# Kernel optimization log

Hardware: AMD Instinct MI355X
Metric: run time of the kernel (lower is better)

Reference implementation:

```python
import jax, jax.numpy as jnp
import numpy as np

INIT_RANGE = 0.02


def setup_inputs() -> dict:
    key = jax.random.key(0)
    ks = jax.random.split(key, 7)
    B, S, E, H, D = 4, 2048, 1024, 16, 64
    return {
        "query": jax.random.normal(ks[0], (B, S, E), dtype=jnp.float32),
        "key": jax.random.normal(ks[1], (B, S, E), dtype=jnp.float32),
        "value": jax.random.normal(ks[2], (B, S, E), dtype=jnp.float32),
        "W_Q": jax.random.normal(ks[3], (H, E, D), dtype=jnp.float32) * INIT_RANGE,
        "W_K": jax.random.normal(ks[4], (H, E, D), dtype=jnp.float32) * INIT_RANGE,
        "W_V": jax.random.normal(ks[5], (H, E, D), dtype=jnp.float32) * INIT_RANGE,
        "W_O": jax.random.normal(ks[6], (H, D, E), dtype=jnp.float32) * INIT_RANGE,
        "b_Q": jnp.zeros((H, D), dtype=jnp.float32),
        "b_K": jnp.zeros((H, D), dtype=jnp.float32),
        "b_V": jnp.zeros((H, D), dtype=jnp.float32),
        "b_O": jnp.zeros((E,), dtype=jnp.float32),
    }


def reference(query, key, value, W_Q, W_K, W_V, W_O, b_Q, b_K, b_V, b_O):
    head_dim = W_Q.shape[-1]
    scale = 1.0 / jnp.sqrt(jnp.asarray(head_dim, dtype=query.dtype))
    # Per-head projections: [B,S,E] x [H,E,D] -> [B,S,H,D]
    Q = jnp.einsum('bse,hed->bshd', query, W_Q) + b_Q
    K = jnp.einsum('bse,hed->bshd', key, W_K) + b_K
    V = jnp.einsum('bse,hed->bshd', value, W_V) + b_V
    # Scores: [B,H,S_from,S_to]
    scores = jnp.einsum('bfhd,bthd->bhft', Q, K) * scale
    attn = jax.nn.softmax(scores, axis=-1)
    # Weighted values: [B,H,S,D]
    OV = jnp.einsum('bhft,bthd->bhfd', attn, V)
    # Output projection: [B,S,E]
    return jnp.einsum('bhsd,hde->bse', OV, W_O) + b_O
```

## Files before the change

kernel.cpp:

```cpp
#include <hip/hip_runtime.h>
#include <hip/hip_bf16.h>

typedef __attribute__((ext_vector_type(8))) short bf16x8;
typedef __attribute__((ext_vector_type(4))) float f32x4;
typedef __attribute__((ext_vector_type(16))) float f32x16;
typedef __attribute__((ext_vector_type(4))) int i32x4;

#define LOG2E 1.4426950408889634f

__device__ __forceinline__ short f2bf(float f){
  unsigned u = __float_as_uint(f);
  u += 0x7fffu + ((u >> 16) & 1u);
  return (short)(u >> 16);
}
__device__ __forceinline__ unsigned cvtpk(float lo, float hi){
  unsigned r;
  asm("v_cvt_pk_bf16_f32 %0, %1, %2" : "=v"(r) : "v"(lo), "v"(hi));
  return r;
}
__device__ __forceinline__ void plswap(unsigned &a, unsigned &b){
  asm("v_permlane32_swap_b32 %0, %1" : "+v"(a), "+v"(b));
}
__device__ __forceinline__ void gl_lds16(const short* g, short* l){
  __builtin_amdgcn_global_load_lds((const __attribute__((address_space(1))) void*)g,
                                   (__attribute__((address_space(3))) void*)l, 16, 0, 0);
}

__global__ __launch_bounds__(256) void prep_wqkv3(const float* __restrict__ Wq,
                                                  const float* __restrict__ Wk,
                                                  const float* __restrict__ Wv,
                                                  short* __restrict__ WqT,
                                                  short* __restrict__ WkT,
                                                  short* __restrict__ WvT){
  __shared__ short t[64][72];
  int h = blockIdx.x >> 4, et = blockIdx.x & 15;
  int tid = threadIdx.x;
  int er = tid >> 2, qc = (tid & 3) * 16;
  #pragma unroll
  for (int a = 0; a < 3; ++a){
    const float* W = a == 0 ? Wq : (a == 1 ? Wk : Wv);
    short* Wt = a == 0 ? WqT : (a == 1 ? WkT : WvT);
    if (a) __syncthreads();
    const float* src = W + h * 65536 + (et * 64 + er) * 64 + qc;
    #pragma unroll
    for (int v = 0; v < 4; ++v){
      float4 f = *(const float4*)(src + v * 4);
      t[qc + v * 4 + 0][er] = f2bf(f.x);
      t[qc + v * 4 + 1][er] = f2bf(f.y);
      t[qc + v * 4 + 2][er] = f2bf(f.z);
      t[qc + v * 4 + 3][er] = f2bf(f.w);
    }
    __syncthreads();
    bf16x8 o0 = *(const bf16x8*)&t[er][qc];
    bf16x8 o1 = *(const bf16x8*)&t[er][qc + 8];
    size_t dst = (size_t)(h * 64 + er) * 1024 + et * 64 + qc;
    *(bf16x8*)&Wt[dst] = o0;
    *(bf16x8*)&Wt[dst + 8] = o1;
  }
}
__global__ __launch_bounds__(256) void prep_wo(const float* __restrict__ W, short* __restrict__ Wt){
  __shared__ short t[64][72];
  int bi = blockIdx.x >> 4, bj = blockIdx.x & 15;
  int tid = threadIdx.x;
  int r = tid >> 2, qc = (tid & 3) * 16;
  const float* src = W + (size_t)(bi * 64 + r) * 1024 + bj * 64 + qc;
  #pragma unroll
  for (int v = 0; v < 4; ++v){
    float4 f = *(const float4*)(src + v * 4);
    t[qc + v * 4 + 0][r] = f2bf(f.x);
    t[qc + v * 4 + 1][r] = f2bf(f.y);
    t[qc + v * 4 + 2][r] = f2bf(f.z);
    t[qc + v * 4 + 3][r] = f2bf(f.w);
  }
  __syncthreads();
  bf16x8 o0 = *(const bf16x8*)&t[r][qc];
  bf16x8 o1 = *(const bf16x8*)&t[r][qc + 8];
  size_t dst = (size_t)(bj * 64 + r) * 1024 + bi * 64 + qc;
  *(bf16x8*)&Wt[dst] = o0;
  *(bf16x8*)&Wt[dst + 8] = o1;
}
__global__ __launch_bounds__(256) void xconv3(const float* __restrict__ xq,
                                              const float* __restrict__ xk,
                                              const float* __restrict__ xv,
                                              short* __restrict__ oq,
                                              short* __restrict__ ok,
                                              short* __restrict__ ov){
  int idx = (blockIdx.x * 256 + threadIdx.x) * 8;
  #pragma unroll
  for (int a = 0; a < 3; ++a){
    const float* x = a == 0 ? xq : (a == 1 ? xk : xv);
    short* o = a == 0 ? oq : (a == 1 ? ok : ov);
    float4 v0 = *(const float4*)&x[idx];
    float4 v1 = *(const float4*)&x[idx + 4];
    bf16x8 t;
    t[0]=f2bf(v0.x); t[1]=f2bf(v0.y); t[2]=f2bf(v0.z); t[3]=f2bf(v0.w);
    t[4]=f2bf(v1.x); t[5]=f2bf(v1.y); t[6]=f2bf(v1.z); t[7]=f2bf(v1.w);
    *(bf16x8*)&o[idx] = t;
  }
}

__global__ __launch_bounds__(256) void proj_gemm(const short* __restrict__ A,
                                                 const short* __restrict__ Wt,
                                                 const float* __restrict__ bias,
                                                 short* __restrict__ Out,
                                                 float scale){
  __shared__ short Al[128][64];
  __shared__ short Bl[128][64];
  int tid = threadIdx.x;
  int bm0 = blockIdx.x * 128, bn0 = blockIdx.y * 128;
  int w = tid >> 6, lane = tid & 63;
  int wm = w >> 1, wn = w & 1;
  int r16 = lane & 15, kblk = lane >> 4;
  int srow = tid >> 3, schunk = tid & 7;

  f32x4 acc[4][4] = {};
  for (int kt = 0; kt < 16; ++kt){
    int k0 = kt * 64;
    __syncthreads();
    #pragma unroll
    for (int p = 0; p < 4; ++p){
      int row = p * 32 + srow;
      int sc = (schunk ^ (row & 7)) * 8;
      gl_lds16(A  + (size_t)(bm0 + row) * 1024 + k0 + sc, &Al[p * 32 + w * 8][0]);
      gl_lds16(Wt + (size_t)(bn0 + row) * 1024 + k0 + sc, &Bl[p * 32 + w * 8][0]);
    }
    __syncthreads();
    bf16x8 af[2][4], bfr[2][4];
    #pragma unroll
    for (int half = 0; half < 2; ++half){
      #pragma unroll
      for (int m = 0; m < 4; ++m){
        int r = wm * 64 + m * 16 + r16;
        af[half][m] = *(bf16x8*)&Al[r][(((half << 2) | kblk) ^ (r & 7)) * 8];
      }
      #pragma unroll
      for (int n = 0; n < 4; ++n){
        int r = wn * 64 + n * 16 + r16;
        bfr[half][n] = *(bf16x8*)&Bl[r][(((half << 2) | kblk) ^ (r & 7)) * 8];
      }
    }
    #pragma unroll
    for (int half = 0; half < 2; ++half)
      #pragma unroll
      for (int m = 0; m < 4; ++m)
        #pragma unroll
        for (int n = 0; n < 4; ++n)
          acc[m][n] = __builtin_amdgcn_mfma_f32_16x16x32_bf16(af[half][m], bfr[half][n], acc[m][n], 0, 0, 0);
  }
  #pragma unroll
  for (int m = 0; m < 4; ++m){
    int grow0 = bm0 + wm * 64 + m * 16 + kblk * 4;
    #pragma unroll
    for (int n = 0; n < 4; ++n){
      int gcol = bn0 + wn * 64 + n * 16 + r16;
      float bv = bias[gcol];
      int h = gcol >> 6, d = gcol & 63;
      #pragma unroll
      for (int i = 0; i < 4; ++i){
        int grow = grow0 + i;
        int b = grow >> 11, s = grow & 2047;
        Out[(size_t)((b * 16 + h) * 2048 + s) * 64 + d] = f2bf((acc[m][n][i] + bv) * scale);
      }
    }
  }
}

__global__ __launch_bounds__(256) void out_gemm(const short* __restrict__ A,
                                                const short* __restrict__ Wt,
                                                const float* __restrict__ bias,
                                                float* __restrict__ Out){
  __shared__ short Al[128][64];
  __shared__ short Bl[128][64];
  int tid = threadIdx.x;
  int bm0 = blockIdx.x * 128, bn0 = blockIdx.y * 128;
  int w = tid >> 6, lane = tid & 63;
  int wm = w >> 1, wn = w & 1;
  int r16 = lane & 15, kblk = lane >> 4;
  int srow = tid >> 3, schunk = tid & 7;
  f32x4 acc[4][4] = {};
  for (int kt = 0; kt < 16; ++kt){
    int k0 = kt * 64;
    __syncthreads();
    #pragma unroll
    for (int p = 0; p < 4; ++p){
      int row = p * 32 + srow;
      int sc = (schunk ^ (row & 7)) * 8;
      gl_lds16(A  + (size_t)(bm0 + row) * 1024 + k0 + sc, &Al[p * 32 + w * 8][0]);
      gl_lds16(Wt + (size_t)(bn0 + row) * 1024 + k0 + sc, &Bl[p * 32 + w * 8][0]);
    }
    __syncthreads();
    bf16x8 af[2][4], bfr[2][4];
    #pragma unroll
    for (int half = 0; half < 2; ++half){
      #pragma unroll
      for (int m = 0; m < 4; ++m){
        int r = wm * 64 + m * 16 + r16;
        af[half][m] = *(bf16x8*)&Al[r][(((half << 2) | kblk) ^ (r & 7)) * 8];
      }
      #pragma unroll
      for (int n = 0; n < 4; ++n){
        int r = wn * 64 + n * 16 + r16;
        bfr[half][n] = *(bf16x8*)&Bl[r][(((half << 2) | kblk) ^ (r & 7)) * 8];
      }
    }
    #pragma unroll
    for (int half = 0; half < 2; ++half)
      #pragma unroll
      for (int m = 0; m < 4; ++m)
        #pragma unroll
        for (int n = 0; n < 4; ++n)
          acc[m][n] = __builtin_amdgcn_mfma_f32_16x16x32_bf16(af[half][m], bfr[half][n], acc[m][n], 0, 0, 0);
  }
  #pragma unroll
  for (int m = 0; m < 4; ++m){
    int grow0 = bm0 + wm * 64 + m * 16 + kblk * 4;
    #pragma unroll
    for (int n = 0; n < 4; ++n){
      int gcol = bn0 + wn * 64 + n * 16 + r16;
      float bv = bias[gcol];
      #pragma unroll
      for (int i = 0; i < 4; ++i)
        Out[(size_t)(grow0 + i) * 1024 + gcol] = acc[m][n][i] + bv;
    }
  }
}

__global__ __launch_bounds__(256) void vtrans(const short* __restrict__ V, short* __restrict__ Vt){
  __shared__ short t[64][68];
  int bh = blockIdx.x >> 5, ts = blockIdx.x & 31;
  int tid = threadIdx.x;
  int r = tid >> 4, c4 = (tid & 15) * 4;
  const short* src = V + ((size_t)bh * 2048 + ts * 64) * 64;
  #pragma unroll
  for (int p = 0; p < 4; ++p){
    int row = p * 16 + r;
    *(short4*)&t[row][c4] = *(const short4*)&src[row * 64 + c4];
  }
  __syncthreads();
  short* dst = Vt + (size_t)bh * 64 * 2048 + ts * 64;
  #pragma unroll
  for (int p = 0; p < 4; ++p){
    int d = p * 16 + r;
    short4 o = make_short4(t[c4 + 0][d], t[c4 + 1][d], t[c4 + 2][d], t[c4 + 3][d]);
    *(short4*)&dst[(size_t)d * 2048 + c4] = o;
  }
}

__device__ __forceinline__ f32x16 mfma32(bf16x8 a, bf16x8 b, f32x16 c){
  return __builtin_amdgcn_mfma_f32_32x32x16_bf16(a, b, c, 0, 0, 0);
}

__device__ __forceinline__ void sm_pack(f32x16& s0, f32x16& s1, float& lrow, bf16x8* pb){
  #pragma unroll
  for (int r = 0; r < 16; ++r) s0[r] = __builtin_amdgcn_exp2f(s0[r]);
  #pragma unroll
  for (int r = 0; r < 16; ++r) s1[r] = __builtin_amdgcn_exp2f(s1[r]);
  float u8_[8];
  #pragma unroll
  for (int r = 0; r < 8; ++r)
    u8_[r] = (s0[r] + s0[r + 8]) + (s1[r] + s1[r + 8]);
  float rs = ((u8_[0] + u8_[1]) + (u8_[2] + u8_[3])) + ((u8_[4] + u8_[5]) + (u8_[6] + u8_[7]));
  rs += __shfl_xor(rs, 32);
  lrow += rs;
  #pragma unroll
  for (int cc = 0; cc < 2; ++cc){
    int b0 = cc * 8;
    unsigned u0 = cvtpk(s0[b0 + 0], s0[b0 + 1]);
    unsigned u1 = cvtpk(s0[b0 + 2], s0[b0 + 3]);
    unsigned w0 = cvtpk(s0[b0 + 4], s0[b0 + 5]);
    unsigned w1 = cvtpk(s0[b0 + 6], s0[b0 + 7]);
    plswap(u0, w0); plswap(u1, w1);
    i32x4 pk0; pk0[0] = (int)u0; pk0[1] = (int)u1; pk0[2] = (int)w0; pk0[3] = (int)w1;
    pb[cc] = __builtin_bit_cast(bf16x8, pk0);
    unsigned y0 = cvtpk(s1[b0 + 0], s1[b0 + 1]);
    unsigned y1 = cvtpk(s1[b0 + 2], s1[b0 + 3]);
    unsigned z0 = cvtpk(s1[b0 + 4], s1[b0 + 5]);
    unsigned z1 = cvtpk(s1[b0 + 6], s1[b0 + 7]);
    plswap(y0, z0); plswap(y1, z1);
    i32x4 pk1; pk1[0] = (int)y0; pk1[1] = (int)y1; pk1[2] = (int)z0; pk1[3] = (int)z1;
    pb[2 + cc] = __builtin_bit_cast(bf16x8, pk1);
  }
}

#define ATT_BODY(T, CUR, NXT)                                                          \
  {                                                                                    \
    if ((T) + 1 < 32){                                                                 \
      _Pragma("unroll")                                                                \
      for (int p = 0; p < 2; ++p){                                                     \
        int row = p * 32 + srow;                                                       \
        gl_lds16(Kp + (size_t)(((T) + 1) * 64 + row) * 64 + sx, &Kl[NXT][p * 32 + w * 8][0]); \
        gl_lds16(Vp + (size_t)row * 2048 + ((T) + 1) * 64 + sx, &Vl[NXT][p * 32 + w * 8][0]); \
      }                                                                                \
    }                                                                                  \
    f32x16 sA0 = {}, sA1 = {}, sB0 = {}, sB1 = {};                                     \
    _Pragma("unroll")                                                                  \
    for (int c = 0; c < 4; ++c){                                                       \
      bf16x8 kf0 = *(const bf16x8*)&Kl[CUR][l31][rchunk[c]];                           \
      bf16x8 kf1 = *(const bf16x8*)&Kl[CUR][32 + l31][rchunk[c]];                      \
      sA0 = mfma32(kf0, qfA[c], sA0);                                                  \
      sA1 = mfma32(kf1, qfA[c], sA1);                                                  \
      sB0 = mfma32(kf0, qfB[c], sB0);                                                  \
      sB1 = mfma32(kf1, qfB[c], sB1);                                                  \
    }                                                                                  \
    bf16x8 pbA[4], pbB[4];                                                             \
    sm_pack(sA0, sA1, lrowA, pbA);                                                     \
    sm_pack(sB0, sB1, lrowB, pbB);                                                     \
    _Pragma("unroll")                                                                  \
    for (int c = 0; c < 4; ++c){                                                       \
      bf16x8 vf0 = *(const bf16x8*)&Vl[CUR][l31][rchunk[c]];                           \
      bf16x8 vf1 = *(const bf16x8*)&Vl[CUR][32 + l31][rchunk[c]];                      \
      accA0 = mfma32(vf0, pbA[c], accA0);                                              \
      accA1 = mfma32(vf1, pbA[c], accA1);                                              \
      accB0 = mfma32(vf0, pbB[c], accB0);                                              \
      accB1 = mfma32(vf1, pbB[c], accB1);                                              \
    }                                                                                  \
    __syncthreads();                                                                   \
  }

__global__ __launch_bounds__(256, 2) void attn(const short* __restrict__ Qb,
                                               const short* __restrict__ Kb,
                                               const short* __restrict__ Vtb,
                                               short* __restrict__ OVb){
  __shared__ short Kl[2][64][64];
  __shared__ short Vl[2][64][64];
  int tid = threadIdx.x;
  int w = tid >> 6, lane = tid & 63;
  int l31 = lane & 31, hi = lane >> 5;
  int bh = blockIdx.x & 63, qb = blockIdx.x >> 6;
  const short* Qp = Qb + ((size_t)bh * 2048 + qb * 256 + w * 64) * 64;
  const short* Kp = Kb + (size_t)bh * 2048 * 64;
  const short* Vp = Vtb + (size_t)bh * 64 * 2048;
  int srow = tid >> 3, schunk = tid & 7;
  int sx = (schunk ^ (srow & 7)) * 8;

  int rchunk[4];
  #pragma unroll
  for (int c = 0; c < 4; ++c) rchunk[c] = (((c << 1) | hi) ^ (l31 & 7)) * 8;

  #pragma unroll
  for (int p = 0; p < 2; ++p){
    int row = p * 32 + srow;
    gl_lds16(Kp + (size_t)row * 64 + sx, &Kl[0][p * 32 + w * 8][0]);
    gl_lds16(Vp + (size_t)row * 2048 + sx, &Vl[0][p * 32 + w * 8][0]);
  }

  bf16x8 qfA[4], qfB[4];
  #pragma unroll
  for (int c = 0; c < 4; ++c){
    qfA[c] = *(const bf16x8*)&Qp[l31 * 64 + c * 16 + hi * 8];
    qfB[c] = *(const bf16x8*)&Qp[(32 + l31) * 64 + c * 16 + hi * 8];
  }

  f32x16 accA0 = {}, accA1 = {}, accB0 = {}, accB1 = {};
  float lrowA = 0.f, lrowB = 0.f;
  __syncthreads();

  for (int t = 0; t < 32; t += 2){
    ATT_BODY(t, 0, 1)
    ATT_BODY(t + 1, 1, 0)
  }

  int b = bh >> 4, h = bh & 15;
  int q0 = qb * 256 + w * 64 + l31;
  float invA = 1.0f / lrowA;
  float invB = 1.0f / lrowB;
  size_t baseA = ((size_t)(b * 2048 + q0)) * 1024 + h * 64;
  size_t baseB = baseA + (size_t)32 * 1024;
  #pragma unroll
  for (int rg = 0; rg < 4; ++rg){
    short4 a0 = make_short4(f2bf(accA0[rg * 4 + 0] * invA), f2bf(accA0[rg * 4 + 1] * invA),
                            f2bf(accA0[rg * 4 + 2] * invA), f2bf(accA0[rg * 4 + 3] * invA));
    *(short4*)&OVb[baseA + rg * 8 + hi * 4] = a0;
    short4 a1 = make_short4(f2bf(accA1[rg * 4 + 0] * invA), f2bf(accA1[rg * 4 + 1] * invA),
                            f2bf(accA1[rg * 4 + 2] * invA), f2bf(accA1[rg * 4 + 3] * invA));
    *(short4*)&OVb[baseA + 32 + rg * 8 + hi * 4] = a1;
    short4 b0 = make_short4(f2bf(accB0[rg * 4 + 0] * invB), f2bf(accB0[rg * 4 + 1] * invB),
                            f2bf(accB0[rg * 4 + 2] * invB), f2bf(accB0[rg * 4 + 3] * invB));
    *(short4*)&OVb[baseB + rg * 8 + hi * 4] = b0;
    short4 b1 = make_short4(f2bf(accB1[rg * 4 + 0] * invB), f2bf(accB1[rg * 4 + 1] * invB),
                            f2bf(accB1[rg * 4 + 2] * invB), f2bf(accB1[rg * 4 + 3] * invB));
    *(short4*)&OVb[baseB + 32 + rg * 8 + hi * 4] = b1;
  }
}

extern "C" void kernel_launch(void* const* d_in, const int* in_sizes, int n_in,
                              void* d_out, int out_size, void* d_ws, size_t ws_size,
                              hipStream_t stream) {
  const float* query = (const float*)d_in[0];
  const float* key_  = (const float*)d_in[1];
  const float* value = (const float*)d_in[2];
  const float* W_Q = (const float*)d_in[3];
  const float* W_K = (const float*)d_in[4];
  const float* W_V = (const float*)d_in[5];
  const float* W_O = (const float*)d_in[6];
  const float* b_Q = (const float*)d_in[7];
  const float* b_K = (const float*)d_in[8];
  const float* b_V = (const float*)d_in[9];
  const float* b_O = (const float*)d_in[10];

  char* ws = (char*)d_ws;
  const size_t MB2 = 2097152, MB16 = 16777216;
  short* WqT = (short*)(ws + 0);
  short* WkT = (short*)(ws + MB2);
  short* WvT = (short*)(ws + 2 * MB2);
  short* WoT = (short*)(ws + 3 * MB2);
  short* RA = (short*)(ws + 4 * MB2);
  short* RB = (short*)(ws + 4 * MB2 + MB16);
  short* RC = (short*)(ws + 4 * MB2 + 2 * MB16);
  short* RD = (short*)(ws + 4 * MB2 + 3 * MB16);
  short* Xq = RA, *Xk = RB, *Xv = RC;
  short* Qb = RD;
  short* Kb = RA;
  short* Vb = RB;
  short* Vtb = RC;
  short* OVb = RB;

  prep_wqkv3<<<256, 256, 0, stream>>>(W_Q, W_K, W_V, WqT, WkT, WvT);
  prep_wo  <<<256, 256, 0, stream>>>(W_O, WoT);
  xconv3   <<<4096, 256, 0, stream>>>(query, key_, value, Xq, Xk, Xv);

  dim3 g(64, 8);
  proj_gemm<<<g, 256, 0, stream>>>(Xq, WqT, b_Q, Qb, LOG2E * 0.125f);
  proj_gemm<<<g, 256, 0, stream>>>(Xk, WkT, b_K, Kb, 1.0f);
  proj_gemm<<<g, 256, 0, stream>>>(Xv, WvT, b_V, Vb, 1.0f);

  vtrans<<<2048, 256, 0, stream>>>(Vb, Vtb);

  attn<<<512, 256, 0, stream>>>(Qb, Kb, Vtb, OVb);

  out_gemm<<<g, 256, 0, stream>>>(OVb, WoT, b_O, (float*)d_out);
}
```

Baseline: 214.3 us.

## Fuse V transpose into projection epilogue and interleave softmax with PV MFMAs

The V projection GEMM now writes its output directly in transposed [B,H,D,S] layout using short4 stores, which removes the separate vtrans kernel and its round trip through memory. Workspace buffer assignments are adjusted to match. In the attention loop, the second softmax/pack is moved between the two halves of the PV MFMA work, and s_setprio raises wave priority around the MFMA sections so that exp/pack work can overlap with matrix ops from other waves. The transposed stores write 8-byte pieces strided across rows, which may coalesce less well than the original epilogue.

```diff
diff --git a/kernel.cpp b/kernel.cpp
--- a/kernel.cpp
+++ b/kernel.cpp
@@ -103,7 +103,7 @@
                                                  const short* __restrict__ Wt,
                                                  const float* __restrict__ bias,
                                                  short* __restrict__ Out,
-                                                 float scale){
+                                                 float scale, int vt_mode){
   __shared__ short Al[128][64];
   __shared__ short Bl[128][64];
   int tid = threadIdx.x;
@@ -147,19 +147,38 @@
         for (int n = 0; n < 4; ++n)
           acc[m][n] = __builtin_amdgcn_mfma_f32_16x16x32_bf16(af[half][m], bfr[half][n], acc[m][n], 0, 0, 0);
   }
-  #pragma unroll
-  for (int m = 0; m < 4; ++m){
-    int grow0 = bm0 + wm * 64 + m * 16 + kblk * 4;
-    #pragma unroll
-    for (int n = 0; n < 4; ++n){
-      int gcol = bn0 + wn * 64 + n * 16 + r16;
-      float bv = bias[gcol];
-      int h = gcol >> 6, d = gcol & 63;
-      #pragma unroll
-      for (int i = 0; i < 4; ++i){
-        int grow = grow0 + i;
-        int b = grow >> 11, s = grow & 2047;
-        Out[(size_t)((b * 16 + h) * 2048 + s) * 64 + d] = f2bf((acc[m][n][i] + bv) * scale);
+  if (!vt_mode){
+    #pragma unroll
+    for (int m = 0; m < 4; ++m){
+      int grow0 = bm0 + wm * 64 + m * 16 + kblk * 4;
+      #pragma unroll
+      for (int n = 0; n < 4; ++n){
+        int gcol = bn0 + wn * 64 + n * 16 + r16;
+        float bv = bias[gcol];
+        int h = gcol >> 6, d = gcol & 63;
+        #pragma unroll
+        for (int i = 0; i < 4; ++i){
+          int grow = grow0 + i;
+          int b = grow >> 11, s = grow & 2047;
+          Out[(size_t)((b * 16 + h) * 2048 + s) * 64 + d] = f2bf((acc[m][n][i] + bv) * scale);
+        }
+      }
+    }
+  } else {
+    #pragma unroll
+    for (int m = 0; m < 4; ++m){
+      int grow0 = bm0 + wm * 64 + m * 16 + kblk * 4;
+      int b = grow0 >> 11, s = grow0 & 2047;
+      #pragma unroll
+      for (int n = 0; n < 4; ++n){
+        int gcol = bn0 + wn * 64 + n * 16 + r16;
+        float bv = bias[gcol];
+        int h = gcol >> 6, d = gcol & 63;
+        short4 o = make_short4(f2bf((acc[m][n][0] + bv) * scale),
+                               f2bf((acc[m][n][1] + bv) * scale),
+                               f2bf((acc[m][n][2] + bv) * scale),
+                               f2bf((acc[m][n][3] + bv) * scale));
+        *(short4*)&Out[(size_t)((b * 16 + h) * 64 + d) * 2048 + s] = o;
       }
     }
   }
@@ -225,27 +244,6 @@
   }
 }
 
-__global__ __launch_bounds__(256) void vtrans(const short* __restrict__ V, short* __restrict__ Vt){
-  __shared__ short t[64][68];
-  int bh = blockIdx.x >> 5, ts = blockIdx.x & 31;
-  int tid = threadIdx.x;
-  int r = tid >> 4, c4 = (tid & 15) * 4;
-  const short* src = V + ((size_t)bh * 2048 + ts * 64) * 64;
-  #pragma unroll
-  for (int p = 0; p < 4; ++p){
-    int row = p * 16 + r;
-    *(short4*)&t[row][c4] = *(const short4*)&src[row * 64 + c4];
-  }
-  __syncthreads();
-  short* dst = Vt + (size_t)bh * 64 * 2048 + ts * 64;
-  #pragma unroll
-  for (int p = 0; p < 4; ++p){
-    int d = p * 16 + r;
-    short4 o = make_short4(t[c4 + 0][d], t[c4 + 1][d], t[c4 + 2][d], t[c4 + 3][d]);
-    *(short4*)&dst[(size_t)d * 2048 + c4] = o;
-  }
-}
-
 __device__ __forceinline__ f32x16 mfma32(bf16x8 a, bf16x8 b, f32x16 c){
   return __builtin_amdgcn_mfma_f32_32x32x16_bf16(a, b, c, 0, 0, 0);
 }
@@ -293,6 +291,7 @@
       }                                                                                \
     }                                                                                  \
     f32x16 sA0 = {}, sA1 = {}, sB0 = {}, sB1 = {};                                     \
+    __builtin_amdgcn_s_setprio(1);                                                     \
     _Pragma("unroll")                                                                  \
     for (int c = 0; c < 4; ++c){                                                       \
       bf16x8 kf0 = *(const bf16x8*)&Kl[CUR][l31][rchunk[c]];                           \
@@ -302,18 +301,27 @@
       sB0 = mfma32(kf0, qfB[c], sB0);                                                  \
       sB1 = mfma32(kf1, qfB[c], sB1);                                                  \
     }                                                                                  \
+    __builtin_amdgcn_s_setprio(0);                                                     \
     bf16x8 pbA[4], pbB[4];                                                             \
     sm_pack(sA0, sA1, lrowA, pbA);                                                     \
-    sm_pack(sB0, sB1, lrowB, pbB);                                                     \
+    bf16x8 vf0_[4], vf1_[4];                                                           \
+    __builtin_amdgcn_s_setprio(1);                                                     \
     _Pragma("unroll")                                                                  \
     for (int c = 0; c < 4; ++c){                                                       \
-      bf16x8 vf0 = *(const bf16x8*)&Vl[CUR][l31][rchunk[c]];                           \
-      bf16x8 vf1 = *(const bf16x8*)&Vl[CUR][32 + l31][rchunk[c]];                      \
-      accA0 = mfma32(vf0, pbA[c], accA0);                                              \
-      accA1 = mfma32(vf1, pbA[c], accA1);                                              \
-      accB0 = mfma32(vf0, pbB[c], accB0);                                              \
-      accB1 = mfma32(vf1, pbB[c], accB1);                                              \
+      vf0_[c] = *(const bf16x8*)&Vl[CUR][l31][rchunk[c]];                              \
+      vf1_[c] = *(const bf16x8*)&Vl[CUR][32 + l31][rchunk[c]];                         \
+      accA0 = mfma32(vf0_[c], pbA[c], accA0);                                          \
+      accA1 = mfma32(vf1_[c], pbA[c], accA1);                                          \
     }                                                                                  \
+    __builtin_amdgcn_s_setprio(0);                                                     \
+    sm_pack(sB0, sB1, lrowB, pbB);                                                     \
+    __builtin_amdgcn_s_setprio(1);                                                     \
+    _Pragma("unroll")                                                                  \
+    for (int c = 0; c < 4; ++c){                                                       \
+      accB0 = mfma32(vf0_[c], pbB[c], accB0);                                          \
+      accB1 = mfma32(vf1_[c], pbB[c], accB1);                                          \
+    }                                                                                  \
+    __builtin_amdgcn_s_setprio(0);                                                     \
     __syncthreads();                                                                   \
   }
 
@@ -411,20 +419,17 @@
   short* Xq = RA, *Xk = RB, *Xv = RC;
   short* Qb = RD;
   short* Kb = RA;
-  short* Vb = RB;
-  short* Vtb = RC;
-  short* OVb = RB;
+  short* Vtb = RB;
+  short* OVb = RC;
 
   prep_wqkv3<<<256, 256, 0, stream>>>(W_Q, W_K, W_V, WqT, WkT, WvT);
   prep_wo  <<<256, 256, 0, stream>>>(W_O, WoT);
   xconv3   <<<4096, 256, 0, stream>>>(query, key_, value, Xq, Xk, Xv);
 
   dim3 g(64, 8);
-  proj_gemm<<<g, 256, 0, stream>>>(Xq, WqT, b_Q, Qb, LOG2E * 0.125f);
-  proj_gemm<<<g, 256, 0, stream>>>(Xk, WkT, b_K, Kb, 1.0f);
-  proj_gemm<<<g, 256, 0, stream>>>(Xv, WvT, b_V, Vb, 1.0f);
-
-  vtrans<<<2048, 256, 0, stream>>>(Vb, Vtb);
+  proj_gemm<<<g, 256, 0, stream>>>(Xq, WqT, b_Q, Qb, LOG2E * 0.125f, 0);
+  proj_gemm<<<g, 256, 0, stream>>>(Xk, WkT, b_K, Kb, 1.0f, 0);
+  proj_gemm<<<g, 256, 0, stream>>>(Xv, WvT, b_V, Vtb, 1.0f, 1);
 
   attn<<<512, 256, 0, stream>>>(Qb, Kb, Vtb, OVb);
 
```

New measurement: 209.4 us. 2.3% less time.
